# Performance work log

Measured on AMD Instinct MI355X. Metric: run time of the kernel, lower is better.

The kernel has to match this reference:

```python
import jax, jax.numpy as jnp
import numpy as np

B, N, DIM, H = 2, 4096, 512, 8
DH = DIM // H  # head dim = 64


def setup_inputs() -> dict:
    key = jax.random.key(0)
    kx, kw, kb = jax.random.split(key, 3)
    x = jax.random.normal(kx, (B, N, DIM), dtype=jnp.float32)
    W = jax.random.normal(kw, (DIM, 3 * DIM), dtype=jnp.float32) / np.sqrt(DIM)
    b = jax.random.normal(kb, (3 * DIM,), dtype=jnp.float32) * 0.02
    return {"x": x, "W": W, "b": b}


def reference(x, W, b):
    Bx, n, d = x.shape
    qvk = x @ W + b  # [B, n, 3*dim]
    # torch.chunk order in source: q, v, k
    q, v, k = jnp.split(qvk, 3, axis=-1)

    def heads(t):  # [B, n, dim] -> [B, h, n, dh]
        return t.reshape(Bx, n, H, DH).transpose(0, 2, 1, 3)

    q, v, k = heads(q), heads(v), heads(k)
    # full (non-fused) attention: materializes [B, h, n, n] scores
    scale = jnp.einsum('bhqd,bhkd->bhqk', q, k) / jnp.sqrt(jnp.float32(DH))
    atn = jax.nn.softmax(scale, axis=-1)
    out = jnp.einsum('bhqk,bhkd->bhqd', atn, v)  # [B, h, n, dh]
    # concat_head: [B, h, n, dh] -> [B, n, h*dh]
    out = out.transpose(0, 2, 1, 3).reshape(Bx, n, H * DH)
    return out
```

## Files before the change

kernel.cpp:

```cpp
#include <hip/hip_runtime.h>
#include <hip/hip_bf16.h>
#include <math.h>

#define BB    2
#define NN    4096
#define DIM   512
#define NH    8
#define DH    64
#define NC    1536
#define MM    (BB*NN)

typedef __bf16 bf16x8 __attribute__((ext_vector_type(8)));
typedef __bf16 bf16x4 __attribute__((ext_vector_type(4)));
typedef float  f32x4  __attribute__((ext_vector_type(4)));

#define QSCALE 0.18033688011112042f

__device__ __forceinline__ int swz(int c) { return c ^ (((c >> 3) ^ (c >> 6)) & 7); }
__device__ __forceinline__ int kswz(int g) { return g ^ ((g >> 3) & 3) ^ (((g >> 6) & 1) << 2); }

__device__ __forceinline__ void gl_lds16(const __hip_bfloat16* g, __bf16* l) {
    __builtin_amdgcn_global_load_lds(
        (const __attribute__((address_space(1))) unsigned int*)g,
        (__attribute__((address_space(3))) unsigned int*)l, 16, 0, 0);
}

__device__ __forceinline__ int sniff(const unsigned short* x) {
    unsigned short v = x[2 * (threadIdx.x & 63)];
    int e = (v >> 7) & 0xFF;
    unsigned long long m = __ballot(e >= 110 && e <= 140);
    return __popcll(m) >= 48;
}

__device__ __forceinline__ f32x4 mfma32(bf16x8 a, bf16x8 b, f32x4 c) {
    return __builtin_amdgcn_mfma_f32_16x16x32_bf16(a, b, c, 0, 0, 0);
}

__global__ __launch_bounds__(256) void prep_kernel(
    const void* __restrict__ xin, const void* __restrict__ win,
    const void* __restrict__ bin,
    __hip_bfloat16* __restrict__ Xb, __hip_bfloat16* __restrict__ WT,
    float* __restrict__ Bf)
{
    __shared__ __bf16 tile[64][68];
    int bfmode = sniff((const unsigned short*)xin);
    int bid = blockIdx.x;
    int t = threadIdx.x;
    if (bid < 2048) {
        if (bfmode) return;
        int i = (bid * 256 + t) * 8;
        const float* xf = (const float*)xin + i;
        bf16x8 v;
        for (int j = 0; j < 8; j++) v[j] = (__bf16)xf[j];
        *(bf16x8*)(Xb + i) = v;
    } else if (bid < 2048 + 192) {
        int tl = bid - 2048;
        int kt = tl / 24, nt = tl % 24;
        int tx = t & 63, tyq = t >> 6;
        for (int r = 0; r < 16; r++) {
            int kl = r * 4 + tyq;
            int gi = (kt * 64 + kl) * NC + nt * 64 + tx;
            float v = bfmode ? __bfloat162float(((const __hip_bfloat16*)win)[gi])
                             : ((const float*)win)[gi];
            tile[kl][tx] = (__bf16)v;
        }
        __syncthreads();
        for (int r = 0; r < 16; r++) {
            int nl = r * 4 + tyq;
            WT[(size_t)(nt * 64 + nl) * DIM + kt * 64 + tx] = (__hip_bfloat16)(float)tile[tx][nl];
        }
    } else {
        int i = (bid - 2048 - 192) * 256 + t;
        if (i < NC)
            Bf[i] = bfmode ? __bfloat162float(((const __hip_bfloat16*)bin)[i])
                           : ((const float*)bin)[i];
    }
}

__global__ __launch_bounds__(256, 3) void qkv_gemm(
    const unsigned short* __restrict__ xs,
    const __hip_bfloat16* __restrict__ Xb,
    const __hip_bfloat16* __restrict__ WT,
    const float* __restrict__ Bf,
    __hip_bfloat16* __restrict__ Qb,
    __hip_bfloat16* __restrict__ Kb,
    __hip_bfloat16* __restrict__ Vt)
{
    __shared__ __align__(16) __bf16 smem[16384];
    __bf16* Xs = smem;
    __bf16* Ws = smem + 8192;

    int bfmode = sniff(xs);
    const __hip_bfloat16* X = bfmode ? (const __hip_bfloat16*)xs : Xb;

    int wave = threadIdx.x >> 6, lane = threadIdx.x & 63;
    int lane16 = lane & 15, quad = lane >> 4;
    int bm = blockIdx.x / 12, bn = blockIdx.x % 12;
    int m0b = bm * 128, n0b = bn * 128;
    int wm = wave >> 1, wn = wave & 1;
    int m0 = m0b + wm * 64, n0 = n0b + wn * 64;

    int xgo[2], sbase[2];
    for (int j = 0; j < 2; j++) {
        int p = (wave * 2 + j) * 64 + lane;
        int g = swz(p);
        xgo[j] = (g >> 2) * DIM + (g & 3) * 8;
        sbase[j] = (wave * 2 + j) * 512;
    }
    int aoff[4], boff[4];
    for (int mi = 0; mi < 4; mi++)
        aoff[mi] = swz((wm * 64 + mi * 16 + lane16) * 4 + quad) * 8;
    for (int ni = 0; ni < 4; ni++)
        boff[ni] = swz((wn * 64 + ni * 16 + lane16) * 4 + quad) * 8;

    const __hip_bfloat16* Xg = X  + (size_t)m0b * DIM;
    const __hip_bfloat16* Wg = WT + (size_t)n0b * DIM;

    for (int j = 0; j < 2; j++) {
        gl_lds16(Xg + xgo[j], &Xs[sbase[j]]);
        gl_lds16(Wg + xgo[j], &Ws[sbase[j]]);
    }
    __syncthreads();

    f32x4 acc[4][4] = {};
    for (int k0 = 0; k0 < DIM; k0 += 32) {
        int cur = (k0 >> 5) & 1, nbuf = cur ^ 1;
        int k1 = (k0 + 32) & (DIM - 1);
        for (int j = 0; j < 2; j++) {
            gl_lds16(Xg + k1 + xgo[j], &Xs[nbuf * 4096 + sbase[j]]);
            gl_lds16(Wg + k1 + xgo[j], &Ws[nbuf * 4096 + sbase[j]]);
        }
        bf16x8 a[4], b[4];
        for (int mi = 0; mi < 4; mi++) a[mi] = *(const bf16x8*)&Xs[cur * 4096 + aoff[mi]];
        for (int ni = 0; ni < 4; ni++) b[ni] = *(const bf16x8*)&Ws[cur * 4096 + boff[ni]];
        for (int mi = 0; mi < 4; mi++)
            for (int ni = 0; ni < 4; ni++)
                acc[mi][ni] = mfma32(a[mi], b[ni], acc[mi][ni]);
        __syncthreads();
    }
    __bf16* epi = smem + wave * 4096;

    int sec = n0b >> 9;
    int bidx = m0b >> 12;
    if (sec == 1) {
        for (int ni = 0; ni < 4; ni++) {
            int nloc = ni * 16 + lane16;
            float bv = Bf[n0 + nloc];
            for (int mi = 0; mi < 4; mi++) {
                bf16x4 pk;
                for (int r = 0; r < 4; r++) pk[r] = (__bf16)(acc[mi][ni][r] + bv);
                int idx = swz(nloc * 8 + mi * 2 + (quad >> 1)) * 8 + (quad & 1) * 4;
                *(bf16x4*)&epi[idx] = pk;
            }
        }
        int hl = (n0 - 512) >> 6;
        int mbase = m0b - bidx * NN + wm * 64;
        for (int p = 0; p < 8; p++) {
            int n = p * 8 + (lane >> 3), mc = lane & 7;
            bf16x8 vv = *(const bf16x8*)&epi[swz(n * 8 + mc) * 8];
            *(bf16x8*)(Vt + ((size_t)(bidx * 8 + hl) * 64 + n) * NN + mbase + mc * 8) = vv;
        }
    } else {
        bool isQ = (sec == 0);
        int h = (n0 & 511) >> 6;
        for (int mi = 0; mi < 4; mi++) {
            for (int ni = 0; ni < 4; ni++) {
                float bv = Bf[n0 + ni * 16 + lane16];
                int dl = ni * 16 + lane16;
                for (int r = 0; r < 4; r++) {
                    int row = mi * 16 + quad * 4 + r;
                    float v = acc[mi][ni][r] + bv;
                    if (isQ) v *= QSCALE;
                    epi[swz(row * 8 + (dl >> 3)) * 8 + (dl & 7)] = (__bf16)v;
                }
            }
        }
        __hip_bfloat16* dst = isQ ? Qb : Kb;
        int bh = bidx * 8 + h;
        int mbase = m0 - bidx * NN;
        for (int p = 0; p < 8; p++) {
            int row = p * 8 + (lane >> 3), dc = lane & 7;
            bf16x8 vv = *(const bf16x8*)&epi[swz(row * 8 + dc) * 8];
            *(bf16x8*)(dst + ((size_t)bh * NN + mbase + row) * DH + dc * 8) = vv;
        }
    }
}

__global__ __launch_bounds__(256, 4) void attn_fused(
    const __hip_bfloat16* __restrict__ Qb,
    const __hip_bfloat16* __restrict__ Kb,
    const __hip_bfloat16* __restrict__ Vt,
    void* __restrict__ OutV,
    const unsigned short* __restrict__ xs)
{
    __shared__ __align__(16) __bf16 smem[16384];

    int bfmode = sniff(xs);
    int wave = threadIdx.x >> 6, lane = threadIdx.x & 63;
    int lane16 = lane & 15, quad = lane >> 4;
    int half = wave >> 1, qw = wave & 1;

    int orig = blockIdx.x;
    int nbid = (orig & 7) * 128 + (orig >> 3);
    int bh = nbid >> 6;
    int qt = nbid & 63;
    int q0 = qt * 64 + qw * 32;
    int khbase = half * 2048;

    __bf16* Kst = smem + half * 8192;
    __bf16* Vst = smem + half * 8192 + 4096;

    const __hip_bfloat16* Qh = Qb + (size_t)bh * NN * DH;
    const __hip_bfloat16* Kh = Kb + (size_t)bh * NN * DH;
    const __hip_bfloat16* Vh = Vt + (size_t)bh * DH * NN;

    bf16x8 bq[2][2];
    #pragma unroll
    for (int qf = 0; qf < 2; qf++)
        #pragma unroll
        for (int kc = 0; kc < 2; kc++)
            bq[qf][kc] = *(const bf16x8*)(Qh + (size_t)(q0 + qf * 16 + lane16) * DH + kc * 32 + quad * 8);

    int kgo[2], vgo[2], sbase[2];
    #pragma unroll
    for (int j = 0; j < 2; j++) {
        int p = (qw * 2 + j) * 64 + lane;
        int gk = kswz(p);
        kgo[j] = (gk >> 3) * DH + (gk & 7) * 8;
        int gv = swz(p);
        vgo[j] = (gv >> 2) * NN + (gv & 3) * 8;
        sbase[j] = (qw * 2 + j) * 512;
    }
    int koff[2][2];
    #pragma unroll
    for (int kf = 0; kf < 2; kf++) {
        int key = (lane16 >> 2) * 8 + 4 * kf + (lane16 & 3);
        #pragma unroll
        for (int kc = 0; kc < 2; kc++)
            koff[kf][kc] = kswz(key * 8 + kc * 4 + quad) * 8;
    }
    int voff[4];
    #pragma unroll
    for (int dt = 0; dt < 4; dt++)
        voff[dt] = swz((dt * 16 + lane16) * 4 + quad) * 8;

    for (int j = 0; j < 2; j++) {
        gl_lds16(Kh + (size_t)khbase * DH + kgo[j], &Kst[sbase[j]]);
        gl_lds16(Vh + khbase + vgo[j], &Vst[sbase[j]]);
    }
    __syncthreads();

    bf16x8 ones8;
    #pragma unroll
    for (int j = 0; j < 8; j++) ones8[j] = (__bf16)1.0f;
    f32x4 o[4][2] = {};
    f32x4 ol[2] = {};

    for (int it = 0; it < 64; ++it) {
        int cur = it & 1, nb = cur ^ 1;
        int k1 = khbase + ((it + 1) & 63) * 32;
        for (int j = 0; j < 2; j++) {
            gl_lds16(Kh + (size_t)k1 * DH + kgo[j], &Kst[nb * 2048 + sbase[j]]);
            gl_lds16(Vh + k1 + vgo[j], &Vst[nb * 2048 + sbase[j]]);
        }

        bf16x8 ka[2][2];
        #pragma unroll
        for (int kf = 0; kf < 2; kf++)
            #pragma unroll
            for (int kc = 0; kc < 2; kc++)
                ka[kf][kc] = *(const bf16x8*)&Kst[cur * 2048 + koff[kf][kc]];
        f32x4 s[2][2];
        #pragma unroll
        for (int kf = 0; kf < 2; kf++)
            #pragma unroll
            for (int qf = 0; qf < 2; qf++) {
                f32x4 t = {};
                t = mfma32(ka[kf][0], bq[qf][0], t);
                t = mfma32(ka[kf][1], bq[qf][1], t);
                s[kf][qf] = t;
            }

        bf16x4 pt[2][2];
        #pragma unroll
        for (int kf = 0; kf < 2; kf++)
            #pragma unroll
            for (int qf = 0; qf < 2; qf++)
                #pragma unroll
                for (int r = 0; r < 4; r++)
                    pt[kf][qf][r] = (__bf16)__builtin_amdgcn_exp2f(s[kf][qf][r]);

        bf16x8 av[4];
        #pragma unroll
        for (int dt = 0; dt < 4; dt++)
            av[dt] = *(const bf16x8*)&Vst[cur * 2048 + voff[dt]];
        #pragma unroll
        for (int qf = 0; qf < 2; qf++) {
            bf16x8 pb = __builtin_shufflevector(pt[0][qf], pt[1][qf],
                                                0, 1, 2, 3, 4, 5, 6, 7);
            #pragma unroll
            for (int dt = 0; dt < 4; dt++)
                o[dt][qf] = mfma32(av[dt], pb, o[dt][qf]);
            ol[qf] = mfma32(ones8, pb, ol[qf]);
        }

        __syncthreads();
    }

    float* Osh = (float*)smem;
    float* lsh = Osh + 2 * 32 * 68;
    if (half == 1) {
        #pragma unroll
        for (int qf = 0; qf < 2; qf++) {
            #pragma unroll
            for (int dt = 0; dt < 4; dt++)
                *(f32x4*)&Osh[(qw * 32 + qf * 16 + lane16) * 68 + dt * 16 + quad * 4] = o[dt][qf];
            if (quad == 0) lsh[qw * 32 + qf * 16 + lane16] = ol[qf][0];
        }
    }
    __syncthreads();
    if (half == 0) {
        __bf16* epi = smem + 8832 + qw * 2048;
        #pragma unroll
        for (int qf = 0; qf < 2; qf++) {
            float l = ol[qf][0] + lsh[qw * 32 + qf * 16 + lane16];
            float rinv = 1.0f / l;
            #pragma unroll
            for (int dt = 0; dt < 4; dt++) {
                f32x4 po = *(const f32x4*)&Osh[(qw * 32 + qf * 16 + lane16) * 68 + dt * 16 + quad * 4];
                #pragma unroll
                for (int r = 0; r < 4; r++) {
                    int d = dt * 16 + quad * 4 + r;
                    int row = qf * 16 + lane16;
                    epi[swz(row * 8 + (d >> 3)) * 8 + (d & 7)] = (__bf16)((o[dt][qf][r] + po[r]) * rinv);
                }
            }
        }
        int bidx = bh >> 3, h = bh & 7;
        for (int p = 0; p < 4; p++) {
            int row = p * 8 + (lane >> 3), mc = lane & 7;
            bf16x8 vv = *(const bf16x8*)&epi[swz(row * 8 + mc) * 8];
            size_t base = ((size_t)bidx * NN + q0 + row) * DIM + h * 64 + mc * 8;
            if (bfmode) {
                *(bf16x8*)((__hip_bfloat16*)OutV + base) = vv;
            } else {
                float* op = (float*)OutV + base;
                f32x4 f0, f1;
                for (int j = 0; j < 4; j++) { f0[j] = (float)vv[j]; f1[j] = (float)vv[4 + j]; }
                *(f32x4*)op = f0;
                *(f32x4*)(op + 4) = f1;
            }
        }
    }
}

extern "C" void kernel_launch(void* const* d_in, const int* in_sizes, int n_in,
                              void* d_out, int out_size, void* d_ws, size_t ws_size,
                              hipStream_t stream) {
    char* ws = (char*)d_ws;
    __hip_bfloat16* Qb = (__hip_bfloat16*)ws;
    __hip_bfloat16* Kb = Qb + (size_t)BB * NH * NN * DH;
    __hip_bfloat16* Vt = Kb + (size_t)BB * NH * NN * DH;
    __hip_bfloat16* WT = Vt + (size_t)BB * NH * NN * DH;
    __hip_bfloat16* Xb = WT + (size_t)NC * DIM;
    float* Bf = (float*)(Xb + (size_t)MM * DIM);

    prep_kernel<<<2048 + 192 + 6, 256, 0, stream>>>(d_in[0], d_in[1], d_in[2], Xb, WT, Bf);
    qkv_gemm<<<(MM / 128) * (NC / 128), 256, 0, stream>>>(
        (const unsigned short*)d_in[0], Xb, WT, Bf, Qb, Kb, Vt);
    attn_fused<<<1024, 256, 0, stream>>>(Qb, Kb, Vt, d_out, (const unsigned short*)d_in[0]);
}
```

Baseline: 182.3 us.

## Load V tiles directly from global into registers, double-buffered, bypassing LDS

Removes the LDS staging of V tiles. Each lane now reads its V fragments straight from global memory into registers, with ping-pong register buffers prefetching the next tile. The loop is unrolled by two via a macro so the buffers alternate statically. This cuts LDS traffic and footprint for V, in exchange for more register pressure and global-load latency that must be hidden within one iteration.

```diff
diff --git a/kernel.cpp b/kernel.cpp
--- a/kernel.cpp
+++ b/kernel.cpp
@@ -207,8 +207,7 @@
     int q0 = qt * 64 + qw * 32;
     int khbase = half * 2048;
 
-    __bf16* Kst = smem + half * 8192;
-    __bf16* Vst = smem + half * 8192 + 4096;
+    __bf16* Kst = smem + half * 4096;
 
     const __hip_bfloat16* Qh = Qb + (size_t)bh * NN * DH;
     const __hip_bfloat16* Kh = Kb + (size_t)bh * NN * DH;
@@ -221,14 +220,12 @@
         for (int kc = 0; kc < 2; kc++)
             bq[qf][kc] = *(const bf16x8*)(Qh + (size_t)(q0 + qf * 16 + lane16) * DH + kc * 32 + quad * 8);
 
-    int kgo[2], vgo[2], sbase[2];
+    int kgo[2], sbase[2];
     #pragma unroll
     for (int j = 0; j < 2; j++) {
         int p = (qw * 2 + j) * 64 + lane;
         int gk = kswz(p);
         kgo[j] = (gk >> 3) * DH + (gk & 7) * 8;
-        int gv = swz(p);
-        vgo[j] = (gv >> 2) * NN + (gv & 3) * 8;
         sbase[j] = (qw * 2 + j) * 512;
     }
     int koff[2][2];
@@ -239,15 +236,15 @@
         for (int kc = 0; kc < 2; kc++)
             koff[kf][kc] = kswz(key * 8 + kc * 4 + quad) * 8;
     }
-    int voff[4];
+    const __hip_bfloat16* Vp = Vh + (size_t)lane16 * NN + quad * 8 + khbase;
+
+    for (int j = 0; j < 2; j++)
+        gl_lds16(Kh + (size_t)khbase * DH + kgo[j], &Kst[sbase[j]]);
+
+    bf16x8 avA[4], avB[4];
     #pragma unroll
     for (int dt = 0; dt < 4; dt++)
-        voff[dt] = swz((dt * 16 + lane16) * 4 + quad) * 8;
-
-    for (int j = 0; j < 2; j++) {
-        gl_lds16(Kh + (size_t)khbase * DH + kgo[j], &Kst[sbase[j]]);
-        gl_lds16(Vh + khbase + vgo[j], &Vst[sbase[j]]);
-    }
+        avA[dt] = *(const bf16x8*)(Vp + (size_t)dt * 16 * NN);
     __syncthreads();
 
     bf16x8 ones8;
@@ -256,56 +253,57 @@
     f32x4 o[4][2] = {};
     f32x4 ol[2] = {};
 
-    for (int it = 0; it < 64; ++it) {
-        int cur = it & 1, nb = cur ^ 1;
-        int k1 = khbase + ((it + 1) & 63) * 32;
-        for (int j = 0; j < 2; j++) {
-            gl_lds16(Kh + (size_t)k1 * DH + kgo[j], &Kst[nb * 2048 + sbase[j]]);
-            gl_lds16(Vh + k1 + vgo[j], &Vst[nb * 2048 + sbase[j]]);
-        }
-
-        bf16x8 ka[2][2];
-        #pragma unroll
-        for (int kf = 0; kf < 2; kf++)
-            #pragma unroll
-            for (int kc = 0; kc < 2; kc++)
-                ka[kf][kc] = *(const bf16x8*)&Kst[cur * 2048 + koff[kf][kc]];
-        f32x4 s[2][2];
-        #pragma unroll
-        for (int kf = 0; kf < 2; kf++)
-            #pragma unroll
-            for (int qf = 0; qf < 2; qf++) {
-                f32x4 t = {};
-                t = mfma32(ka[kf][0], bq[qf][0], t);
-                t = mfma32(ka[kf][1], bq[qf][1], t);
-                s[kf][qf] = t;
-            }
-
-        bf16x4 pt[2][2];
-        #pragma unroll
-        for (int kf = 0; kf < 2; kf++)
-            #pragma unroll
-            for (int qf = 0; qf < 2; qf++)
-                #pragma unroll
-                for (int r = 0; r < 4; r++)
-                    pt[kf][qf][r] = (__bf16)__builtin_amdgcn_exp2f(s[kf][qf][r]);
-
-        bf16x8 av[4];
-        #pragma unroll
-        for (int dt = 0; dt < 4; dt++)
-            av[dt] = *(const bf16x8*)&Vst[cur * 2048 + voff[dt]];
-        #pragma unroll
-        for (int qf = 0; qf < 2; qf++) {
-            bf16x8 pb = __builtin_shufflevector(pt[0][qf], pt[1][qf],
-                                                0, 1, 2, 3, 4, 5, 6, 7);
-            #pragma unroll
-            for (int dt = 0; dt < 4; dt++)
-                o[dt][qf] = mfma32(av[dt], pb, o[dt][qf]);
-            ol[qf] = mfma32(ones8, pb, ol[qf]);
-        }
-
-        __syncthreads();
-    }
+#define AT_STEP(CUR, AVC, AVN, IT)                                                 \
+    {                                                                              \
+        int kn = ((IT) + 1) & 63;                                                  \
+        int k1 = khbase + kn * 32;                                                 \
+        for (int j = 0; j < 2; j++)                                                \
+            gl_lds16(Kh + (size_t)k1 * DH + kgo[j],                                \
+                     &Kst[((CUR) ^ 1) * 2048 + sbase[j]]);                         \
+        _Pragma("unroll")                                                          \
+        for (int dt = 0; dt < 4; dt++)                                             \
+            AVN[dt] = *(const bf16x8*)(Vp + (size_t)dt * 16 * NN + kn * 32);       \
+        bf16x8 ka[2][2];                                                           \
+        _Pragma("unroll")                                                          \
+        for (int kf = 0; kf < 2; kf++)                                             \
+            _Pragma("unroll")                                                      \
+            for (int kc = 0; kc < 2; kc++)                                         \
+                ka[kf][kc] = *(const bf16x8*)&Kst[(CUR) * 2048 + koff[kf][kc]];    \
+        f32x4 s[2][2];                                                             \
+        _Pragma("unroll")                                                          \
+        for (int kf = 0; kf < 2; kf++)                                             \
+            _Pragma("unroll")                                                      \
+            for (int qf = 0; qf < 2; qf++) {                                       \
+                f32x4 t = {};                                                      \
+                t = mfma32(ka[kf][0], bq[qf][0], t);                               \
+                t = mfma32(ka[kf][1], bq[qf][1], t);                               \
+                s[kf][qf] = t;                                                     \
+            }                                                                      \
+        bf16x4 pt[2][2];                                                           \
+        _Pragma("unroll")                                                          \
+        for (int kf = 0; kf < 2; kf++)                                             \
+            _Pragma("unroll")                                                      \
+            for (int qf = 0; qf < 2; qf++)                                         \
+                _Pragma("unroll")                                                  \
+                for (int r = 0; r < 4; r++)                                        \
+                    pt[kf][qf][r] = (__bf16)__builtin_amdgcn_exp2f(s[kf][qf][r]);  \
+        _Pragma("unroll")                                                          \
+        for (int qf = 0; qf < 2; qf++) {                                           \
+            bf16x8 pb = __builtin_shufflevector(pt[0][qf], pt[1][qf],              \
+                                                0, 1, 2, 3, 4, 5, 6, 7);           \
+            _Pragma("unroll")                                                      \
+            for (int dt = 0; dt < 4; dt++)                                         \
+                o[dt][qf] = mfma32(AVC[dt], pb, o[dt][qf]);                        \
+            ol[qf] = mfma32(ones8, pb, ol[qf]);                                    \
+        }                                                                          \
+        __syncthreads();                                                           \
+    }
+
+    for (int it = 0; it < 64; it += 2) {
+        AT_STEP(0, avA, avB, it);
+        AT_STEP(1, avB, avA, it + 1);
+    }
+#undef AT_STEP
 
     float* Osh = (float*)smem;
     float* lsh = Osh + 2 * 32 * 68;
```

Measured after the change: 257.5 us. 1.41x slower.
